# Kernel tuning notes

Measured on AMD Instinct MI355X. Metric: run time of the kernel, lower is better.

The kernel has to match this reference:

```python
import jax, jax.numpy as jnp
import numpy as np

B, T, C, H = 8, 2048, 1024, 128


def setup_inputs() -> dict:
    key = jax.random.key(0)
    k1, k2, k3, k4 = jax.random.split(key, 4)
    x = jax.random.normal(k1, (B, T, C), dtype=jnp.float32)
    # Linear(n_embd, head_size, bias=False): weight is [head_size, n_embd] in torch,
    # applied as x @ W.T; we store W already transposed as [C, H].
    s = 1.0 / np.sqrt(C)
    Wk = jax.random.normal(k2, (C, H), dtype=jnp.float32) * s
    Wq = jax.random.normal(k3, (C, H), dtype=jnp.float32) * s
    Wv = jax.random.normal(k4, (C, H), dtype=jnp.float32) * s
    return {"x": x, "Wk": Wk, "Wq": Wq, "Wv": Wv}


def reference(x, Wk, Wq, Wv):
    # k, q, v projections
    k = jnp.einsum("btc,ch->bth", x, Wk)
    q = jnp.einsum("btc,ch->bth", x, Wq)
    v = jnp.einsum("btc,ch->bth", x, Wv)
    scale = k.shape[-1] ** -0.5
    wei = jnp.einsum("bqh,bkh->bqk", q, k) * scale  # [B,T,T]
    # causal mask: tril == 0 -> -inf
    Tq = x.shape[1]
    causal = jnp.tril(jnp.ones((Tq, Tq), dtype=bool))
    wei = jnp.where(causal, wei, -jnp.inf)
    wei = jax.nn.softmax(wei, axis=-1)
    # dropout p=0.0 -> identity
    out = jnp.einsum("bqk,bkh->bqh", wei, v)  # [B,T,H]
    return out
```

## Files before the change

kernel.cpp:

```cpp
#include <hip/hip_runtime.h>

typedef unsigned short u16;
typedef __attribute__((ext_vector_type(8))) short bf16x8;
typedef __attribute__((ext_vector_type(4))) float f32x4;
typedef __attribute__((ext_vector_type(4))) unsigned int u32x4;
typedef __attribute__((ext_vector_type(2))) unsigned int u32x2;

#define MFMA16(a, b, c) __builtin_amdgcn_mfma_f32_16x16x32_bf16((a), (b), (c), 0, 0, 0)

static constexpr int Bn = 8, Tn = 2048, Cn = 1024, Hn = 128;

static __device__ __forceinline__ u16 f2bf(float f) {
  union { float f; unsigned u; } v;
  v.f = f;
  unsigned r = v.u + 0x7fffu + ((v.u >> 16) & 1u);
  return (u16)(r >> 16);
}

static __device__ __forceinline__ float bf2f(u16 h) {
  union { unsigned u; float f; } v;
  v.u = ((unsigned)h) << 16;
  return v.f;
}

static __device__ __forceinline__ unsigned pack2(float a, float b) {
  return (unsigned)f2bf(a) | ((unsigned)f2bf(b) << 16);
}

__global__ __launch_bounds__(256) void wt_kernel(const float* __restrict__ Wk,
                                                 const float* __restrict__ Wq,
                                                 const float* __restrict__ Wv,
                                                 u16* __restrict__ Wt) {
  __shared__ u16 tile[64][65];
  const int c0 = blockIdx.x * 64;
  const int h0 = blockIdx.y * 64;
  const int z = blockIdx.z;
  const float* W = (z == 0) ? Wk : (z == 1) ? Wq : Wv;
  u16* dst = Wt + (size_t)z * Hn * Cn;
  const int tx = threadIdx.x & 63;
  const int ty = threadIdx.x >> 6;
#pragma unroll
  for (int i = 0; i < 16; ++i) {
    int r = ty * 16 + i;
    tile[r][tx] = f2bf(W[(size_t)(c0 + r) * Hn + h0 + tx]);
  }
  __syncthreads();
#pragma unroll
  for (int i = 0; i < 16; ++i) {
    int r = ty * 16 + i;
    dst[(size_t)(h0 + r) * Cn + c0 + tx] = tile[tx][r];
  }
}

__global__ __launch_bounds__(512, 4) void proj_kernel(const float* __restrict__ X,
                                                      const u16* __restrict__ Wt,
                                                      u16* __restrict__ Kb,
                                                      u16* __restrict__ Qb,
                                                      u16* __restrict__ Vt) {
  __shared__ u16 Xs[64][72];
  __shared__ u16 Ws[384][72];

  const int m0 = blockIdx.x * 64;
  const int tid = threadIdx.x;
  const int w = tid >> 6;
  const int wm = w & 1;
  const int wh = w >> 1;
  const int lane = tid & 63;
  const int l15 = lane & 15, lg = lane >> 4;

  const int xr = tid >> 3;
  const int xc = (tid & 7) * 8;
  const float* xptr = X + (size_t)(m0 + xr) * Cn + xc;
  const u16* wptr = Wt + (size_t)xr * Cn + xc;

  f32x4 acc[6][2] = {};
  f32x4 xl0, xl1;
  bf16x8 wl[6];

  xl0 = *reinterpret_cast<const f32x4*>(xptr);
  xl1 = *reinterpret_cast<const f32x4*>(xptr + 4);
#pragma unroll
  for (int i = 0; i < 6; ++i)
    wl[i] = *reinterpret_cast<const bf16x8*>(wptr + (size_t)i * 64 * Cn);

  for (int kt = 0; kt < Cn; kt += 64) {
    __syncthreads();
    {
      union { u16 h[8]; bf16x8 v; } cv;
#pragma unroll
      for (int j = 0; j < 4; ++j) {
        cv.h[j] = f2bf(xl0[j]);
        cv.h[4 + j] = f2bf(xl1[j]);
      }
      *reinterpret_cast<bf16x8*>(&Xs[xr][xc]) = cv.v;
#pragma unroll
      for (int i = 0; i < 6; ++i)
        *reinterpret_cast<bf16x8*>(&Ws[xr + i * 64][xc]) = wl[i];
    }
    if (kt + 64 < Cn) {
      xl0 = *reinterpret_cast<const f32x4*>(xptr + kt + 64);
      xl1 = *reinterpret_cast<const f32x4*>(xptr + kt + 64 + 4);
#pragma unroll
      for (int i = 0; i < 6; ++i)
        wl[i] = *reinterpret_cast<const bf16x8*>(wptr + (size_t)i * 64 * Cn + kt + 64);
    }
    __syncthreads();
#pragma unroll
    for (int kk = 0; kk < 2; ++kk) {
      const int ko = kk * 32 + lg * 8;
      bf16x8 af[6], bfx[2];
#pragma unroll
      for (int hf = 0; hf < 6; ++hf)
        af[hf] = *reinterpret_cast<const bf16x8*>(&Ws[wh * 96 + hf * 16 + l15][ko]);
#pragma unroll
      for (int mf = 0; mf < 2; ++mf)
        bfx[mf] = *reinterpret_cast<const bf16x8*>(&Xs[wm * 32 + mf * 16 + l15][ko]);
#pragma unroll
      for (int hf = 0; hf < 6; ++hf)
#pragma unroll
        for (int mf = 0; mf < 2; ++mf)
          acc[hf][mf] = MFMA16(af[hf], bfx[mf], acc[hf][mf]);
    }
  }

#pragma unroll
  for (int hf = 0; hf < 6; ++hf) {
    const int habs = wh * 96 + hf * 16 + lg * 4;
    const int p = habs >> 7;
    const int h = habs & 127;
    const float sc = (p == 1) ? 0.08838834764831845f : 1.0f;
#pragma unroll
    for (int mf = 0; mf < 2; ++mf) {
      const int m = m0 + wm * 32 + mf * 16 + l15;
      union { u16 h4[4]; u32x2 v; } pk;
#pragma unroll
      for (int r = 0; r < 4; ++r) pk.h4[r] = f2bf(acc[hf][mf][r] * sc);
      if (p == 0) {
        *reinterpret_cast<u32x2*>(&Kb[(size_t)m * Hn + h]) = pk.v;
      } else if (p == 1) {
        *reinterpret_cast<u32x2*>(&Qb[(size_t)m * Hn + h]) = pk.v;
      } else {
        const int b = m >> 11, t = m & (Tn - 1);
#pragma unroll
        for (int r = 0; r < 4; ++r)
          Vt[((size_t)b * Hn + h + r) * Tn + t] = pk.h4[r];
      }
    }
  }
}

__global__ __launch_bounds__(512) void attn_kernel(const u16* __restrict__ Qb,
                                                   const u16* __restrict__ Kb,
                                                   const u16* __restrict__ Vt,
                                                   float* __restrict__ Out) {
  __shared__ u16 SM[78848];
  __shared__ float Ml[8][16][2];

  const int batch = blockIdx.x & 7;
  const int rrank = blockIdx.x >> 3;
  const int q0 = (31 - rrank) << 6;
  const int tid = threadIdx.x;
  const int w = tid >> 6;
  const int sw = w >> 1;
  const int par = w & 1;
  const int lane = tid & 63;
  const int l15 = lane & 15, lg = lane >> 4;

  const size_t bt = (size_t)batch * Tn;
  const int qrow = q0 + sw * 16;
  const int q = qrow + l15;

  bf16x8 qb[4];
#pragma unroll
  for (int kk = 0; kk < 4; ++kk)
    qb[kk] = *reinterpret_cast<const bf16x8*>(&Qb[(bt + q) * Hn + kk * 32 + lg * 8]);

  f32x4 o[8] = {};
  float m_r = -1e30f;
  float l_r = 0.f;

  const int nt = (q0 + 64 + 127) >> 7;

  u32x4 kreg[4], vreg[4];
#define ATTN_LOAD(KN)                                                          \
  _Pragma("unroll")                                                            \
  for (int i = 0; i < 4; ++i) {                                                \
    const int idx = tid + i * 512;                                             \
    const int row = idx >> 4, c8 = (idx & 15) * 8;                             \
    kreg[i] = *reinterpret_cast<const u32x4*>(&Kb[(bt + (KN) + row) * Hn + c8]); \
    vreg[i] = *reinterpret_cast<const u32x4*>(                                 \
        &Vt[((size_t)batch * Hn + row) * Tn + (KN) + c8]);                     \
  }

#define ATTN_STAGE(BUF)                                                        \
  _Pragma("unroll")                                                            \
  for (int i = 0; i < 4; ++i) {                                                \
    const int idx = tid + i * 512;                                             \
    const int row = idx >> 4, c8 = (idx & 15) * 8;                             \
    *reinterpret_cast<u32x4*>(&SM[(BUF) * 34816 + row * 136 + c8]) = kreg[i];  \
    *reinterpret_cast<u32x4*>(&SM[(BUF) * 34816 + 17408 + row * 136 + c8]) = vreg[i]; \
  }

  ATTN_LOAD(0)
  ATTN_STAGE(0)
  if (nt > 1) ATTN_LOAD(128)
  __syncthreads();

  for (int t = 0; t < nt; ++t) {
    const int cur = t & 1;
    const int k0 = t << 7;
    const int kbase = k0 + par * 64;
    if (kbase <= qrow) {
      const u16* KsB = &SM[cur * 34816];
      const u16* VsB = &SM[cur * 34816 + 17408];
      f32x4 s[4] = {};
#pragma unroll
      for (int nf = 0; nf < 4; ++nf) {
#pragma unroll
        for (int kk = 0; kk < 4; ++kk) {
          bf16x8 ka = *reinterpret_cast<const bf16x8*>(
              &KsB[(par * 64 + nf * 16 + l15) * 136 + kk * 32 + lg * 8]);
          s[nf] = MFMA16(ka, qb[kk], s[nf]);
        }
      }

      if (kbase + 63 > qrow) {
#pragma unroll
        for (int nf = 0; nf < 4; ++nf)
#pragma unroll
          for (int r = 0; r < 4; ++r)
            if (kbase + nf * 16 + lg * 4 + r > q) s[nf][r] = -1e30f;
      }

      float mx = -1e30f;
#pragma unroll
      for (int nf = 0; nf < 4; ++nf)
#pragma unroll
        for (int r = 0; r < 4; ++r) mx = fmaxf(mx, s[nf][r]);
      mx = fmaxf(mx, __shfl_xor(mx, 16));
      mx = fmaxf(mx, __shfl_xor(mx, 32));
      const float mn = fmaxf(m_r, mx);
      const float scv = __expf(m_r - mn);
      float rs = 0.f;
#pragma unroll
      for (int nf = 0; nf < 4; ++nf)
#pragma unroll
        for (int r = 0; r < 4; ++r) {
          s[nf][r] = __expf(s[nf][r] - mn);
          rs += s[nf][r];
        }
      rs += __shfl_xor(rs, 16);
      rs += __shfl_xor(rs, 32);
      l_r = l_r * scv + rs;
      m_r = mn;
#pragma unroll
      for (int n = 0; n < 8; ++n) o[n] *= scv;

      u16* PlW = &SM[69632 + w * 1152];
#pragma unroll
      for (int nf = 0; nf < 4; ++nf) {
        u32x2 pv;
        pv.x = pack2(s[nf][0], s[nf][1]);
        pv.y = pack2(s[nf][2], s[nf][3]);
        *reinterpret_cast<u32x2*>(&PlW[l15 * 72 + nf * 16 + lg * 4]) = pv;
      }
      asm volatile("s_waitcnt lgkmcnt(0)" ::: "memory");
      __builtin_amdgcn_sched_barrier(0);
      bf16x8 pb[2];
#pragma unroll
      for (int ks = 0; ks < 2; ++ks)
        pb[ks] = *reinterpret_cast<const bf16x8*>(&PlW[l15 * 72 + ks * 32 + lg * 8]);

#pragma unroll
      for (int n = 0; n < 8; ++n) {
#pragma unroll
        for (int ks = 0; ks < 2; ++ks) {
          bf16x8 va = *reinterpret_cast<const bf16x8*>(
              &VsB[(n * 16 + l15) * 136 + par * 64 + ks * 32 + lg * 8]);
          o[n] = MFMA16(va, pb[ks], o[n]);
        }
      }
    }

    if (t + 1 < nt) {
      ATTN_STAGE(cur ^ 1)
      if (t + 2 < nt) ATTN_LOAD((t + 2) << 7)
    }
    __syncthreads();
  }

#pragma unroll
  for (int n = 0; n < 8; ++n) {
    u32x2 ov;
    ov.x = pack2(o[n][0], o[n][1]);
    ov.y = pack2(o[n][2], o[n][3]);
    *reinterpret_cast<u32x2*>(&SM[w * 2176 + l15 * 136 + n * 16 + lg * 4]) = ov;
  }
  if (lg == 0) {
    Ml[w][l15][0] = m_r;
    Ml[w][l15][1] = l_r;
  }
  __syncthreads();

  {
    const int row = tid >> 3;
    const int h0 = (tid & 7) * 16;
    const int s_ = row >> 4;
    const int r16 = row & 15;
    const int w0 = s_ * 2, w1 = w0 + 1;
    const float m0v = Ml[w0][r16][0], l0v = Ml[w0][r16][1];
    const float m1v = Ml[w1][r16][0], l1v = Ml[w1][r16][1];
    const float M = fmaxf(m0v, m1v);
    const float e0 = __expf(m0v - M), e1 = __expf(m1v - M);
    const float inv = 1.0f / (l0v * e0 + l1v * e1);
    const u16* Oa = &SM[w0 * 2176 + r16 * 136 + h0];
    const u16* Ob = &SM[w1 * 2176 + r16 * 136 + h0];
    u32x4 a0 = *reinterpret_cast<const u32x4*>(Oa);
    u32x4 a1 = *reinterpret_cast<const u32x4*>(Oa + 8);
    u32x4 b0 = *reinterpret_cast<const u32x4*>(Ob);
    u32x4 b1 = *reinterpret_cast<const u32x4*>(Ob + 8);
    float outv[16];
#pragma unroll
    for (int j = 0; j < 4; ++j) {
      outv[2 * j]     = (e0 * bf2f((u16)(a0[j] & 0xffffu)) + e1 * bf2f((u16)(b0[j] & 0xffffu))) * inv;
      outv[2 * j + 1] = (e0 * bf2f((u16)(a0[j] >> 16))     + e1 * bf2f((u16)(b0[j] >> 16))) * inv;
      outv[8 + 2 * j]     = (e0 * bf2f((u16)(a1[j] & 0xffffu)) + e1 * bf2f((u16)(b1[j] & 0xffffu))) * inv;
      outv[8 + 2 * j + 1] = (e0 * bf2f((u16)(a1[j] >> 16))     + e1 * bf2f((u16)(b1[j] >> 16))) * inv;
    }
    float* op = &Out[(bt + q0 + row) * Hn + h0];
#pragma unroll
    for (int j = 0; j < 4; ++j)
      *reinterpret_cast<f32x4*>(op + j * 4) = *reinterpret_cast<const f32x4*>(&outv[j * 4]);
  }
}

extern "C" void kernel_launch(void* const* d_in, const int* in_sizes, int n_in,
                              void* d_out, int out_size, void* d_ws, size_t ws_size,
                              hipStream_t stream) {
  const float* X = (const float*)d_in[0];
  const float* Wk = (const float*)d_in[1];
  const float* Wq = (const float*)d_in[2];
  const float* Wv = (const float*)d_in[3];

  char* ws = (char*)d_ws;
  u16* Wt = (u16*)(ws);
  u16* Kb = (u16*)(ws + 786432);
  u16* Qb = (u16*)(ws + 786432 + 4194304);
  u16* Vt = (u16*)(ws + 786432 + 2 * 4194304);
  float* Out = (float*)d_out;

  wt_kernel<<<dim3(16, 2, 3), 256, 0, stream>>>(Wk, Wq, Wv, Wt);
  proj_kernel<<<dim3(256), 512, 0, stream>>>(X, Wt, Kb, Qb, Vt);
  attn_kernel<<<dim3(Bn * 32), 512, 0, stream>>>(Qb, Kb, Vt, Out);
}
```

Measured before the change: 73.37 us.

## Halve attention query tile to 32 rows and use single-buffered LDS

The attention kernel now handles 32 query rows per block with 4 waves (256 threads) instead of 64 rows with 8 waves. The grid grows to 512 blocks, and the causal work is spread more finely across blocks. The double-buffered K/V LDS tiles are replaced by one buffer fed from a register prefetch, with two barriers per tile. This halves shared memory per block so more blocks can be resident per CU. In exchange, each K/V tile is loaded by twice as many blocks, and the extra barrier adds synchronisation per tile.

```diff
diff --git a/kernel.cpp b/kernel.cpp
--- a/kernel.cpp
+++ b/kernel.cpp
@@ -149,16 +149,18 @@
   }
 }
 
-__global__ __launch_bounds__(512) void attn_kernel(const u16* __restrict__ Qb,
+__global__ __launch_bounds__(256) void attn_kernel(const u16* __restrict__ Qb,
                                                    const u16* __restrict__ Kb,
                                                    const u16* __restrict__ Vt,
                                                    float* __restrict__ Out) {
-  __shared__ u16 SM[78848];
-  __shared__ float Ml[8][16][2];
+  __shared__ u16 SM[39424];
+  __shared__ float Ml[4][16][2];
+  constexpr int VOFF = 17408;
+  constexpr int PLOFF = 34816;
 
   const int batch = blockIdx.x & 7;
-  const int rrank = blockIdx.x >> 3;
-  const int q0 = (31 - rrank) << 6;
+  const int sr = blockIdx.x >> 3;
+  const int q0 = (63 - sr) << 5;
   const int tid = threadIdx.x;
   const int w = tid >> 6;
   const int sw = w >> 1;
@@ -179,47 +181,45 @@
   float m_r = -1e30f;
   float l_r = 0.f;
 
-  const int nt = (q0 + 64 + 127) >> 7;
-
-  u32x4 kreg[4], vreg[4];
+  const int nt = (q0 + 32 + 127) >> 7;
+
+  u32x4 kreg[8], vreg[8];
 #define ATTN_LOAD(KN)                                                          \
   _Pragma("unroll")                                                            \
-  for (int i = 0; i < 4; ++i) {                                                \
-    const int idx = tid + i * 512;                                             \
-    const int row = idx >> 4, c8 = (idx & 15) * 8;                             \
-    kreg[i] = *reinterpret_cast<const u32x4*>(&Kb[(bt + (KN) + row) * Hn + c8]); \
+  for (int i = 0; i < 8; ++i) {                                                \
+    const int idx = tid + i * 256;                                             \
+    const int kr = idx >> 4, kc = (idx & 15) * 8;                              \
+    kreg[i] = *reinterpret_cast<const u32x4*>(&Kb[(bt + (KN) + kr) * Hn + kc]); \
     vreg[i] = *reinterpret_cast<const u32x4*>(                                 \
-        &Vt[((size_t)batch * Hn + row) * Tn + (KN) + c8]);                     \
-  }
-
-#define ATTN_STAGE(BUF)                                                        \
+        &Vt[((size_t)batch * Hn + kr) * Tn + (KN) + kc]);                      \
+  }
+
+#define ATTN_STAGE()                                                           \
   _Pragma("unroll")                                                            \
-  for (int i = 0; i < 4; ++i) {                                                \
-    const int idx = tid + i * 512;                                             \
-    const int row = idx >> 4, c8 = (idx & 15) * 8;                             \
-    *reinterpret_cast<u32x4*>(&SM[(BUF) * 34816 + row * 136 + c8]) = kreg[i];  \
-    *reinterpret_cast<u32x4*>(&SM[(BUF) * 34816 + 17408 + row * 136 + c8]) = vreg[i]; \
+  for (int i = 0; i < 8; ++i) {                                                \
+    const int idx = tid + i * 256;                                             \
+    const int kr = idx >> 4, kc = (idx & 15) * 8;                              \
+    *reinterpret_cast<u32x4*>(&SM[kr * 136 + kc]) = kreg[i];                   \
+    *reinterpret_cast<u32x4*>(&SM[VOFF + kr * 136 + kc]) = vreg[i];            \
   }
 
   ATTN_LOAD(0)
-  ATTN_STAGE(0)
-  if (nt > 1) ATTN_LOAD(128)
-  __syncthreads();
 
   for (int t = 0; t < nt; ++t) {
-    const int cur = t & 1;
+    __syncthreads();
+    ATTN_STAGE()
+    if (t + 1 < nt) ATTN_LOAD((t + 1) << 7)
+    __syncthreads();
     const int k0 = t << 7;
     const int kbase = k0 + par * 64;
     if (kbase <= qrow) {
-      const u16* KsB = &SM[cur * 34816];
-      const u16* VsB = &SM[cur * 34816 + 17408];
       f32x4 s[4] = {};
 #pragma unroll
       for (int nf = 0; nf < 4; ++nf) {
 #pragma unroll
         for (int kk = 0; kk < 4; ++kk) {
           bf16x8 ka = *reinterpret_cast<const bf16x8*>(
-              &KsB[(par * 64 + nf * 16 + l15) * 136 + kk * 32 + lg * 8]);
+              &SM[(par * 64 + nf * 16 + l15) * 136 + kk * 32 + lg * 8]);
           s[nf] = MFMA16(ka, qb[kk], s[nf]);
         }
       }
@@ -256,7 +256,7 @@
 #pragma unroll
       for (int n = 0; n < 8; ++n) o[n] *= scv;
 
-      u16* PlW = &SM[69632 + w * 1152];
+      u16* PlW = &SM[PLOFF + w * 1152];
 #pragma unroll
       for (int nf = 0; nf < 4; ++nf) {
         u32x2 pv;
@@ -276,18 +276,14 @@
 #pragma unroll
         for (int ks = 0; ks < 2; ++ks) {
           bf16x8 va = *reinterpret_cast<const bf16x8*>(
-              &VsB[(n * 16 + l15) * 136 + par * 64 + ks * 32 + lg * 8]);
+              &SM[VOFF + (n * 16 + l15) * 136 + par * 64 + ks * 32 + lg * 8]);
           o[n] = MFMA16(va, pb[ks], o[n]);
         }
       }
     }
-
-    if (t + 1 < nt) {
-      ATTN_STAGE(cur ^ 1)
-      if (t + 2 < nt) ATTN_LOAD((t + 2) << 7)
-    }
-    __syncthreads();
-  }
+  }
+
+  __syncthreads();
 
 #pragma unroll
   for (int n = 0; n < 8; ++n) {
@@ -351,5 +347,5 @@
 
   wt_kernel<<<dim3(16, 2, 3), 256, 0, stream>>>(Wk, Wq, Wv, Wt);
   proj_kernel<<<dim3(256), 512, 0, stream>>>(X, Wt, Kb, Qb, Vt);
-  attn_kernel<<<dim3(Bn * 32), 512, 0, stream>>>(Qb, Kb, Vt, Out);
-}
+  attn_kernel<<<dim3(512), 256, 0, stream>>>(Qb, Kb, Vt, Out);
+}
```

New measurement: 73.77 us. Within noise of the previous version (+0.5%).
